# Kernel optimization log

Measured on AMD Instinct MI355X. Metric: run time of the kernel, lower is better.

## Reference

```python
import jax, jax.numpy as jnp
import numpy as np

N_NODES = 50000
N_EDGES = 800000
D_IN = 64
D_HID = 128  # out_channels * expansion(2)
EPS_MSG = 1e-7
EPS_SOFTMAX = 1e-16
EPS_BN = 1e-5
N_LAYERS = 4


def mish(x):
    return x * jnp.tanh(jax.nn.softplus(x))


def setup_inputs() -> dict:
    key = jax.random.key(0)
    ks = jax.random.split(key, 8)
    x = jax.random.normal(ks[0], (N_NODES, D_IN), dtype=jnp.float32)
    edge_index = jax.random.randint(ks[1], (2, N_EDGES), 0, N_NODES, dtype=jnp.int64)
    # Per-layer GENConv MLP params: Linear(64->128), BN(128), ReLU, Linear(128->64)
    s1 = 1.0 / np.sqrt(D_IN)
    s2 = 1.0 / np.sqrt(D_HID)
    W1 = jax.random.uniform(ks[2], (N_LAYERS, D_IN, D_HID), jnp.float32, -s1, s1)
    b1 = jax.random.uniform(ks[3], (N_LAYERS, D_HID), jnp.float32, -s1, s1)
    gamma = jnp.ones((N_LAYERS, D_HID), jnp.float32)
    beta = jnp.zeros((N_LAYERS, D_HID), jnp.float32)
    W2 = jax.random.uniform(ks[4], (N_LAYERS, D_HID, D_IN), jnp.float32, -s2, s2)
    b2 = jax.random.uniform(ks[5], (N_LAYERS, D_IN), jnp.float32, -s2, s2)
    return {"x": x, "edge_index": edge_index, "W1": W1, "b1": b1,
            "gamma": gamma, "beta": beta, "W2": W2, "b2": b2}


def gen_conv(x, src, dst, W1, b1, gamma, beta, W2, b2):
    n = x.shape[0]
    # message: relu(x_j) + eps  -> [E, D]
    msg = jax.nn.relu(x[src]) + EPS_MSG
    # softmax aggregation (t=1) per destination node, per feature channel
    m = jax.ops.segment_max(msg, dst, num_segments=n)
    e = jnp.exp(msg - m[dst])
    denom = jax.ops.segment_sum(e, dst, num_segments=n)[dst] + EPS_SOFTMAX
    alpha = e / denom
    agg = jax.ops.segment_sum(msg * alpha, dst, num_segments=n)
    # residual with destination features, then 2-layer MLP w/ BatchNorm (train mode)
    h = agg + x
    h = h @ W1 + b1
    mu = jnp.mean(h, axis=0)
    var = jnp.var(h, axis=0)  # biased, as torch BN uses for normalization
    h = (h - mu) * jax.lax.rsqrt(var + EPS_BN) * gamma + beta
    h = jax.nn.relu(h)
    return h @ W2 + b2


def reference(x, edge_index, W1, b1, gamma, beta, W2, b2):
    src, dst = edge_index[0], edge_index[1]
    h = x
    for i in range(N_LAYERS):
        h = gen_conv(h, src, dst, W1[i], b1[i], gamma[i], beta[i], W2[i], b2[i])
        if i < N_LAYERS - 1:
            h = mish(h)
    return h
```

## Files before the change

### kernel.cpp

```cpp
#include <hip/hip_runtime.h>
#include <math.h>

#define N_NODES 50000
#define N_EDGES 800000
#define D_IN 64
#define D_HID 128
#define SCAN_B 256
#define N_SB ((N_NODES + SCAN_B - 1) / SCAN_B)
#define NPB 256
#define NB ((N_NODES + NPB - 1) / NPB)
#define P1_BLOCKS 256
#define EPB (N_EDGES / P1_BLOCKS)

typedef unsigned short u16;
typedef unsigned int u32;
typedef __attribute__((ext_vector_type(8))) short short8;
typedef __attribute__((ext_vector_type(4))) float f32x4;

union U4S8 { uint4 u; short8 s; };

__device__ __forceinline__ float bf2f(u16 u) {
    u32 x = ((u32)u) << 16;
    float f; __builtin_memcpy(&f, &x, 4); return f;
}
__device__ __forceinline__ u16 f2bf(float f) {
    u32 x; __builtin_memcpy(&x, &f, 4);
    x += 0x7fffu + ((x >> 16) & 1u);
    return (u16)(x >> 16);
}
__device__ __forceinline__ u32 pk2(float a, float b) {
    return (u32)f2bf(a) | ((u32)f2bf(b) << 16);
}
__device__ __forceinline__ u32 relu2(u32 w) {
    u32 b = (w >> 15) & 0x00010001u;
    u32 m01 = b ^ 0x00010001u;
    u32 M = (m01 << 16) - m01;
    return w & M;
}


__global__ void count_kernel(const int* __restrict__ dst, int* __restrict__ deg, int E) {
    int i = blockIdx.x * blockDim.x + threadIdx.x;
    if (i < E) atomicAdd(&deg[dst[i]], 1);
}

__global__ __launch_bounds__(SCAN_B) void scan_reduce_kernel(const int* __restrict__ deg,
                                                             int* __restrict__ bsum) {
    __shared__ int s[SCAN_B];
    int i = blockIdx.x * SCAN_B + threadIdx.x;
    int v = (i < N_NODES) ? deg[i] : 0;
    s[threadIdx.x] = v;
    __syncthreads();
    #pragma unroll
    for (int o = SCAN_B / 2; o > 0; o >>= 1) {
        if (threadIdx.x < o) s[threadIdx.x] += s[threadIdx.x + o];
        __syncthreads();
    }
    if (threadIdx.x == 0) bsum[blockIdx.x] = s[0];
}

__global__ __launch_bounds__(SCAN_B) void scan_sums_kernel(const int* __restrict__ bsum,
                                                           int* __restrict__ boff) {
    __shared__ int s[SCAN_B];
    int t = threadIdx.x;
    int v = (t < N_SB) ? bsum[t] : 0;
    s[t] = v;
    __syncthreads();
    #pragma unroll
    for (int o = 1; o < SCAN_B; o <<= 1) {
        int u = (t >= o) ? s[t - o] : 0;
        __syncthreads();
        s[t] += u;
        __syncthreads();
    }
    if (t < N_SB) boff[t] = s[t] - v;
}

__global__ __launch_bounds__(SCAN_B) void scan_write_kernel(const int* __restrict__ deg,
                                                            const int* __restrict__ boff,
                                                            int* __restrict__ off) {
    __shared__ int s[SCAN_B];
    int t = threadIdx.x;
    int i = blockIdx.x * SCAN_B + t;
    int v = (i < N_NODES) ? deg[i] : 0;
    s[t] = v;
    __syncthreads();
    #pragma unroll
    for (int o = 1; o < SCAN_B; o <<= 1) {
        int u = (t >= o) ? s[t - o] : 0;
        __syncthreads();
        s[t] += u;
        __syncthreads();
    }
    int incl = s[t] + boff[blockIdx.x];
    if (i < N_NODES) off[i] = incl - v;
    if (i == N_NODES - 1) off[N_NODES] = incl;
}

__global__ void bin_init_kernel(const int* __restrict__ off, int* __restrict__ gcur,
                                int* __restrict__ esrc) {
    int b = threadIdx.x;
    if (b < NB) gcur[b] = off[min(b * NPB, N_NODES)];
    if (b < 16) esrc[N_EDGES + b] = 0;
}

__global__ __launch_bounds__(256) void bin_pass1_kernel(const int* __restrict__ src,
                                                        const int* __restrict__ dst,
                                                        int* __restrict__ gcur,
                                                        int2* __restrict__ ebuf) {
    __shared__ int hist[NB];
    __shared__ int base[NB];
    const int tid = threadIdx.x;
    const int e0 = blockIdx.x * EPB, e1 = e0 + EPB;
    for (int b = tid; b < NB; b += 256) hist[b] = 0;
    __syncthreads();
    for (int i = e0 + tid; i < e1; i += 256)
        atomicAdd(&hist[dst[i] >> 8], 1);
    __syncthreads();
    for (int b = tid; b < NB; b += 256) {
        base[b] = atomicAdd(&gcur[b], hist[b]);
        hist[b] = 0;
    }
    __syncthreads();
    for (int i = e0 + tid; i < e1; i += 256) {
        int d = dst[i];
        int b = d >> 8;
        int slot = base[b] + atomicAdd(&hist[b], 1);
        ebuf[slot] = make_int2(src[i], d);
    }
}

__global__ __launch_bounds__(256) void bin_pass2_kernel(const int* __restrict__ off,
                                                        const int2* __restrict__ ebuf,
                                                        int* __restrict__ esrc) {
    __shared__ int soff[NPB];
    __shared__ int cur[NPB];
    const int b = blockIdx.x;
    const int tid = threadIdx.x;
    const int n0 = b * NPB;
    soff[tid] = off[min(n0 + tid, N_NODES)];
    cur[tid] = 0;
    __syncthreads();
    const int e0 = soff[0];
    const int e1 = off[min(n0 + NPB, N_NODES)];
    for (int i = e0 + tid; i < e1; i += 256) {
        int2 p = ebuf[i];
        int dl = p.y - n0;
        int slot = soff[dl] + atomicAdd(&cur[dl], 1);
        esrc[slot] = p.x;
    }
}

__global__ __launch_bounds__(256) void xcvt_kernel(const float* __restrict__ x,
                                                   u16* __restrict__ xb,
                                                   u16* __restrict__ rb) {
    int i = blockIdx.x * 256 + threadIdx.x;
    if (i < N_NODES * D_IN / 4) {
        float4 v = ((const float4*)x)[i];
        u32 lo = pk2(v.x, v.y), hi = pk2(v.z, v.w);
        ((uint2*)xb)[i] = make_uint2(lo, hi);
        ((uint2*)rb)[i] = make_uint2(relu2(lo), relu2(hi));
    }
}

__global__ __launch_bounds__(256) void wprep_kernel(const float* __restrict__ W1,
                                                    const float* __restrict__ W2,
                                                    u16* __restrict__ w1f,
                                                    u16* __restrict__ w2f) {
    const int b = blockIdx.x;
    const int L = b >> 1;
    if ((b & 1) == 0) {
        const float* W = W1 + (size_t)L * 64 * 128;
        u16* outp = w1f + (size_t)L * 8192;
        for (int idx = threadIdx.x; idx < 1024; idx += 256) {
            int ln = idx & 63, th = idx >> 6;
            int half = th & 1, t = th >> 1;
            int k0 = half * 32 + (ln >> 4) * 8;
            int n = t * 16 + (ln & 15);
            uint4 o;
            o.x = pk2(W[(k0 + 0) * 128 + n], W[(k0 + 1) * 128 + n]);
            o.y = pk2(W[(k0 + 2) * 128 + n], W[(k0 + 3) * 128 + n]);
            o.z = pk2(W[(k0 + 4) * 128 + n], W[(k0 + 5) * 128 + n]);
            o.w = pk2(W[(k0 + 6) * 128 + n], W[(k0 + 7) * 128 + n]);
            *(uint4*)&outp[(size_t)idx * 8] = o;
        }
    } else {
        const float* W = W2 + (size_t)L * 128 * 64;
        u16* outp = w2f + (size_t)L * 8192;
        for (int idx = threadIdx.x; idx < 1024; idx += 256) {
            int ln = idx & 63, th = idx >> 6;
            int ks = th & 3, t = th >> 2;
            int k0 = ks * 32 + (ln >> 4) * 8;
            int n = t * 16 + (ln & 15);
            uint4 o;
            o.x = pk2(W[(k0 + 0) * 64 + n], W[(k0 + 1) * 64 + n]);
            o.y = pk2(W[(k0 + 2) * 64 + n], W[(k0 + 3) * 64 + n]);
            o.z = pk2(W[(k0 + 4) * 64 + n], W[(k0 + 5) * 64 + n]);
            o.w = pk2(W[(k0 + 6) * 64 + n], W[(k0 + 7) * 64 + n]);
            *(uint4*)&outp[(size_t)idx * 8] = o;
        }
    }
}

__global__ __launch_bounds__(256) void agg_kernel(const u16* __restrict__ xb,
                                                  const u16* __restrict__ rb,
                                                  const int* __restrict__ off,
                                                  const int* __restrict__ esrc,
                                                  u16* __restrict__ h) {
    const int node = blockIdx.x * 4 + (threadIdx.x >> 6);
    const int ln = threadIdx.x & 63;
    const int jb = __builtin_amdgcn_readfirstlane(off[node]);
    const int je = __builtin_amdgcn_readfirstlane(off[node + 1]);
    const float xown = bf2f(xb[(size_t)node * 64 + ln]);
    float s0 = 0.f, s1 = 0.f, t0 = 0.f, t1 = 0.f;
    int j = jb;
    const int nfull = (je - jb) >> 4;
    for (int it = 0; it < nfull; ++it, j += 16) {
        #pragma unroll
        for (int kk = 0; kk < 16; kk += 2) {
            int i0 = esrc[j + kk];
            int i1 = esrc[j + kk + 1];
            float m0 = bf2f(rb[(size_t)i0 * 64 + ln]);
            float m1 = bf2f(rb[(size_t)i1 * 64 + ln]);
            float p0 = __expf(m0);
            float p1 = __expf(m1);
            s0 += p0; t0 = fmaf(m0, p0, t0);
            s1 += p1; t1 = fmaf(m1, p1, t1);
        }
    }
    const int rem = je - j;
    if (rem > 0) {
        #pragma unroll
        for (int kk = 0; kk < 16; kk += 2) {
            int i0 = esrc[j + kk];
            int i1 = esrc[j + kk + 1];
            float m0 = bf2f(rb[(size_t)i0 * 64 + ln]);
            float m1 = bf2f(rb[(size_t)i1 * 64 + ln]);
            float p0 = (kk < rem)     ? __expf(m0) : 0.f;
            float p1 = (kk + 1 < rem) ? __expf(m1) : 0.f;
            s0 += p0; t0 = fmaf(m0, p0, t0);
            s1 += p1; t1 = fmaf(m1, p1, t1);
        }
    }
    const float s = s0 + s1, t = t0 + t1;
    const float v = t / (s + 1e-16f) + 1e-7f + xown;
    h[(size_t)node * 64 + ln] = f2bf(v);
}

#define SC1 136
__global__ __launch_bounds__(256) void gemm1_kernel(const u16* __restrict__ A,
                                                    const u16* __restrict__ Wf,
                                                    const float* __restrict__ bias,
                                                    u16* __restrict__ Bout,
                                                    float* __restrict__ S,
                                                    float* __restrict__ Q) {
    __shared__ u16 sC[64 * SC1];
    __shared__ float sRed[2][4][128];
    const int tid = threadIdx.x;
    const int wave = tid >> 6, ln = tid & 63;
    const int lm = ln & 15, quad = ln >> 4;
    const int row0g = blockIdx.x * 64;
    const int row0 = row0g + wave * 16;
    const int rA = min(row0 + lm, N_NODES - 1);

    U4S8 a0, a1;
    a0.u = *(const uint4*)&A[(size_t)rA * 64 + quad * 8];
    a1.u = *(const uint4*)&A[(size_t)rA * 64 + 32 + quad * 8];

    f32x4 acc[8];
    #pragma unroll
    for (int t = 0; t < 8; t++) {
        float b = bias[t * 16 + lm];
        acc[t] = (f32x4){b, b, b, b};
    }
    #pragma unroll
    for (int t = 0; t < 8; t++) {
        U4S8 b0, b1;
        b0.u = *(const uint4*)&Wf[(size_t)((t * 2 + 0) * 64 + ln) * 8];
        b1.u = *(const uint4*)&Wf[(size_t)((t * 2 + 1) * 64 + ln) * 8];
        acc[t] = __builtin_amdgcn_mfma_f32_16x16x32_bf16(a0.s, b0.s, acc[t], 0, 0, 0);
        acc[t] = __builtin_amdgcn_mfma_f32_16x16x32_bf16(a1.s, b1.s, acc[t], 0, 0, 0);
    }
    const int rbase = row0 + quad * 4;
    #pragma unroll
    for (int t = 0; t < 8; t++) {
        float ss = 0.f, qq = 0.f;
        #pragma unroll
        for (int rg = 0; rg < 4; rg++) {
            if (rbase + rg < N_NODES) {
                float v = acc[t][rg];
                ss += v; qq = fmaf(v, v, qq);
            }
        }
        ss += __shfl_xor(ss, 16); ss += __shfl_xor(ss, 32);
        qq += __shfl_xor(qq, 16); qq += __shfl_xor(qq, 32);
        if (quad == 0) {
            sRed[0][wave][t * 16 + lm] = ss;
            sRed[1][wave][t * 16 + lm] = qq;
        }
    }
    const int lr0 = wave * 16 + quad * 4;
    #pragma unroll
    for (int t = 0; t < 8; t++) {
        #pragma unroll
        for (int rg = 0; rg < 4; rg++)
            sC[(lr0 + rg) * SC1 + t * 16 + lm] = f2bf(acc[t][rg]);
    }
    __syncthreads();
    const int c8 = (tid & 15) * 8;
    #pragma unroll
    for (int i = 0; i < 4; i++) {
        int lr = (tid >> 4) + i * 16;
        int r = row0g + lr;
        if (r < N_NODES)
            *(uint4*)&Bout[(size_t)r * 128 + c8] = *(const uint4*)&sC[lr * SC1 + c8];
    }
    if (tid < 128) {
        float v = sRed[0][0][tid] + sRed[0][1][tid] + sRed[0][2][tid] + sRed[0][3][tid];
        atomicAdd(&S[tid], v);
    } else {
        int c = tid - 128;
        float v = sRed[1][0][c] + sRed[1][1][c] + sRed[1][2][c] + sRed[1][3][c];
        atomicAdd(&Q[c], v);
    }
}

__device__ __forceinline__ float mish_f(float v) {
    if (v > 30.f) return v;
    float u = __expf(v);
    float t = (u + 1.f) * (u + 1.f);
    return v * (t - 1.f) / (t + 1.f);
}

#define SC2B 72
#define SC2F 68
__global__ __launch_bounds__(256) void gemm2_kernel(const u16* __restrict__ H,
                                                    const float* __restrict__ S,
                                                    const float* __restrict__ Q,
                                                    const float* __restrict__ gamma,
                                                    const float* __restrict__ beta,
                                                    const u16* __restrict__ Wf,
                                                    const float* __restrict__ bias,
                                                    float* __restrict__ outf,
                                                    u16* __restrict__ xb,
                                                    u16* __restrict__ rb,
                                                    int dobf16) {
    __shared__ float sss[256];
    __shared__ __align__(16) char sCraw[64 * SC2F * 4];
    u16* sCb = (u16*)sCraw;
    float* sCf = (float*)sCraw;
    const int tid = threadIdx.x;
    if (tid < 128) {
        float mean = S[tid] * (1.f / N_NODES);
        float var = fmaxf(Q[tid] * (1.f / N_NODES) - mean * mean, 0.f);
        float sc = gamma[tid] * rsqrtf(var + 1e-5f);
        sss[tid] = sc;
        sss[128 + tid] = beta[tid] - mean * sc;
    }
    __syncthreads();
    const int wave = tid >> 6, ln = tid & 63;
    const int lm = ln & 15, quad = ln >> 4;
    const int row0g = blockIdx.x * 64;
    const int row0 = row0g + wave * 16;
    const int rA = min(row0 + lm, N_NODES - 1);

    f32x4 acc[4];
    #pragma unroll
    for (int t = 0; t < 4; t++) {
        float b = bias[t * 16 + lm];
        acc[t] = (f32x4){b, b, b, b};
    }
    #pragma unroll
    for (int ks = 0; ks < 4; ks++) {
        const int k0 = ks * 32 + quad * 8;
        U4S8 h8;
        h8.u = *(const uint4*)&H[(size_t)rA * 128 + k0];
        U4S8 a;
        #pragma unroll
        for (int j2 = 0; j2 < 4; j2++) {
            int k = k0 + 2 * j2;
            float v0 = fmaxf(fmaf(bf2f((u16)h8.s[2 * j2]),     sss[k],     sss[128 + k]),     0.f);
            float v1 = fmaxf(fmaf(bf2f((u16)h8.s[2 * j2 + 1]), sss[k + 1], sss[128 + k + 1]), 0.f);
            ((u32*)&a.u)[j2] = pk2(v0, v1);
        }
        #pragma unroll
        for (int t = 0; t < 4; t++) {
            U4S8 b;
            b.u = *(const uint4*)&Wf[(size_t)((t * 4 + ks) * 64 + ln) * 8];
            acc[t] = __builtin_amdgcn_mfma_f32_16x16x32_bf16(a.s, b.s, acc[t], 0, 0, 0);
        }
    }
    const int lr0 = wave * 16 + quad * 4;
    if (dobf16) {
        #pragma unroll
        for (int t = 0; t < 4; t++) {
            #pragma unroll
            for (int rg = 0; rg < 4; rg++)
                sCb[(lr0 + rg) * SC2B + t * 16 + lm] = f2bf(mish_f(acc[t][rg]));
        }
        __syncthreads();
        const int c8 = (tid & 7) * 8;
        #pragma unroll
        for (int i = 0; i < 2; i++) {
            int lr = (tid >> 3) + i * 32;
            int r = row0g + lr;
            if (r < N_NODES) {
                uint4 val = *(const uint4*)&sCb[lr * SC2B + c8];
                *(uint4*)&xb[(size_t)r * 64 + c8] = val;
                uint4 rv;
                rv.x = relu2(val.x); rv.y = relu2(val.y);
                rv.z = relu2(val.z); rv.w = relu2(val.w);
                *(uint4*)&rb[(size_t)r * 64 + c8] = rv;
            }
        }
    } else {
        #pragma unroll
        for (int t = 0; t < 4; t++) {
            #pragma unroll
            for (int rg = 0; rg < 4; rg++)
                sCf[(lr0 + rg) * SC2F + t * 16 + lm] = acc[t][rg];
        }
        __syncthreads();
        const int c8 = (tid & 7) * 8;
        #pragma unroll
        for (int i = 0; i < 2; i++) {
            int lr = (tid >> 3) + i * 32;
            int r = row0g + lr;
            if (r < N_NODES) {
                *(float4*)&outf[(size_t)r * 64 + c8]     = *(const float4*)&sCf[lr * SC2F + c8];
                *(float4*)&outf[(size_t)r * 64 + c8 + 4] = *(const float4*)&sCf[lr * SC2F + c8 + 4];
            }
        }
    }
}


extern "C" void kernel_launch(void* const* d_in, const int* in_sizes, int n_in,
                              void* d_out, int out_size, void* d_ws, size_t ws_size,
                              hipStream_t stream) {
    const float* x     = (const float*)d_in[0];
    const int*   ei    = (const int*)d_in[1];
    const float* W1    = (const float*)d_in[2];
    const float* b1    = (const float*)d_in[3];
    const float* gamma = (const float*)d_in[4];
    const float* beta  = (const float*)d_in[5];
    const float* W2    = (const float*)d_in[6];
    const float* b2    = (const float*)d_in[7];
    float* out = (float*)d_out;

    const int* src = ei;
    const int* dst = ei + N_EDGES;

    char* base = (char*)d_ws;
    size_t o = 0;
    auto take = [&](size_t bytes) -> char* {
        char* p = base + o;
        o = (o + bytes + 255) & ~(size_t)255;
        return p;
    };
    int* deg     = (int*)take((size_t)N_NODES * 4);
    int* off     = (int*)take((size_t)(N_NODES + 1) * 4);
    int* esrc    = (int*)take((size_t)(N_EDGES + 16) * 4);
    int2* ebuf   = (int2*)take((size_t)N_EDGES * 8);
    int* bsum    = (int*)take((size_t)N_SB * 4);
    int* boff    = (int*)take((size_t)N_SB * 4);
    int* gcur    = (int*)take((size_t)NB * 4);
    float* bn    = (float*)take(1024 * 4);
    u16* w1f     = (u16*)take((size_t)4 * 8192 * 2);
    u16* w2f     = (u16*)take((size_t)4 * 8192 * 2);
    u16* xbuf    = (u16*)take((size_t)N_NODES * D_IN * 2);
    u16* rbuf    = (u16*)take((size_t)N_NODES * D_IN * 2);
    u16* hbuf    = (u16*)take((size_t)N_NODES * D_IN * 2);
    u16* h1buf   = (u16*)take((size_t)N_NODES * D_HID * 2);

    hipMemsetAsync(deg, 0, (size_t)N_NODES * 4, stream);
    hipMemsetAsync(bn, 0, 1024 * 4, stream);
    count_kernel<<<(N_EDGES + 255) / 256, 256, 0, stream>>>(dst, deg, N_EDGES);
    scan_reduce_kernel<<<N_SB, SCAN_B, 0, stream>>>(deg, bsum);
    scan_sums_kernel<<<1, SCAN_B, 0, stream>>>(bsum, boff);
    scan_write_kernel<<<N_SB, SCAN_B, 0, stream>>>(deg, boff, off);
    bin_init_kernel<<<1, 256, 0, stream>>>(off, gcur, esrc);
    bin_pass1_kernel<<<P1_BLOCKS, 256, 0, stream>>>(src, dst, gcur, ebuf);
    bin_pass2_kernel<<<NB, 256, 0, stream>>>(off, ebuf, esrc);
    xcvt_kernel<<<(N_NODES * D_IN / 4 + 255) / 256, 256, 0, stream>>>(x, xbuf, rbuf);
    wprep_kernel<<<8, 256, 0, stream>>>(W1, W2, w1f, w2f);

    const int NBLK = (N_NODES + 63) / 64;
    const int ABLK = (N_NODES + 3) / 4;
    for (int L = 0; L < 4; L++) {
        float* Sb = bn + L * 256;
        float* Qb = Sb + 128;
        agg_kernel<<<ABLK, 256, 0, stream>>>(xbuf, rbuf, off, esrc, hbuf);
        gemm1_kernel<<<NBLK, 256, 0, stream>>>(
            hbuf, w1f + (size_t)L * 8192, b1 + (size_t)L * D_HID, h1buf,
            Sb, Qb);
        gemm2_kernel<<<NBLK, 256, 0, stream>>>(
            h1buf, Sb, Qb, gamma + (size_t)L * D_HID, beta + (size_t)L * D_HID,
            w2f + (size_t)L * 8192, b2 + (size_t)L * D_IN,
            out, xbuf, rbuf, (L < 3) ? 1 : 0);
    }
}
```

Before: 400.6 us.

## Fuse neighbor aggregation into first GEMM and pack binning edge pairs

The separate aggregation kernel is merged into the first GEMM kernel. Each wave now aggregates its 16 rows into LDS, and the MFMA operands are read from LDS, so the intermediate bf16 h buffer and one launch per layer are gone. The binning buffer also packs src and dst into a single 32-bit word instead of an int2, halving that scratch traffic. The cost is much less parallelism in the gather: it drops from 12500 small blocks to about 782 blocks with serial per-wave node loops. That could hurt latency hiding for the random row gathers.

New measurement: 416.6 us. 4.0% more time.

```diff
diff --git a/kernel.cpp b/kernel.cpp
--- a/kernel.cpp
+++ b/kernel.cpp
@@ -107,7 +107,7 @@
 __global__ __launch_bounds__(256) void bin_pass1_kernel(const int* __restrict__ src,
                                                         const int* __restrict__ dst,
                                                         int* __restrict__ gcur,
-                                                        int2* __restrict__ ebuf) {
+                                                        u32* __restrict__ ebuf) {
     __shared__ int hist[NB];
     __shared__ int base[NB];
     const int tid = threadIdx.x;
@@ -126,12 +126,12 @@
         int d = dst[i];
         int b = d >> 8;
         int slot = base[b] + atomicAdd(&hist[b], 1);
-        ebuf[slot] = make_int2(src[i], d);
+        ebuf[slot] = ((u32)src[i] << 16) | (u32)d;
     }
 }
 
 __global__ __launch_bounds__(256) void bin_pass2_kernel(const int* __restrict__ off,
-                                                        const int2* __restrict__ ebuf,
+                                                        const u32* __restrict__ ebuf,
                                                         int* __restrict__ esrc) {
     __shared__ int soff[NPB];
     __shared__ int cur[NPB];
@@ -144,10 +144,10 @@
     const int e0 = soff[0];
     const int e1 = off[min(n0 + NPB, N_NODES)];
     for (int i = e0 + tid; i < e1; i += 256) {
-        int2 p = ebuf[i];
-        int dl = p.y - n0;
+        u32 p = ebuf[i];
+        int dl = (int)(p & 0xFFFFu) - n0;
         int slot = soff[dl] + atomicAdd(&cur[dl], 1);
-        esrc[slot] = p.x;
+        esrc[slot] = (int)(p >> 16);
     }
 }
 
@@ -202,70 +202,75 @@
     }
 }
 
-__global__ __launch_bounds__(256) void agg_kernel(const u16* __restrict__ xb,
-                                                  const u16* __restrict__ rb,
-                                                  const int* __restrict__ off,
-                                                  const int* __restrict__ esrc,
-                                                  u16* __restrict__ h) {
-    const int node = blockIdx.x * 4 + (threadIdx.x >> 6);
-    const int ln = threadIdx.x & 63;
-    const int jb = __builtin_amdgcn_readfirstlane(off[node]);
-    const int je = __builtin_amdgcn_readfirstlane(off[node + 1]);
-    const float xown = bf2f(xb[(size_t)node * 64 + ln]);
-    float s0 = 0.f, s1 = 0.f, t0 = 0.f, t1 = 0.f;
-    int j = jb;
-    const int nfull = (je - jb) >> 4;
-    for (int it = 0; it < nfull; ++it, j += 16) {
-        #pragma unroll
-        for (int kk = 0; kk < 16; kk += 2) {
-            int i0 = esrc[j + kk];
-            int i1 = esrc[j + kk + 1];
-            float m0 = bf2f(rb[(size_t)i0 * 64 + ln]);
-            float m1 = bf2f(rb[(size_t)i1 * 64 + ln]);
-            float p0 = __expf(m0);
-            float p1 = __expf(m1);
-            s0 += p0; t0 = fmaf(m0, p0, t0);
-            s1 += p1; t1 = fmaf(m1, p1, t1);
-        }
-    }
-    const int rem = je - j;
-    if (rem > 0) {
-        #pragma unroll
-        for (int kk = 0; kk < 16; kk += 2) {
-            int i0 = esrc[j + kk];
-            int i1 = esrc[j + kk + 1];
-            float m0 = bf2f(rb[(size_t)i0 * 64 + ln]);
-            float m1 = bf2f(rb[(size_t)i1 * 64 + ln]);
-            float p0 = (kk < rem)     ? __expf(m0) : 0.f;
-            float p1 = (kk + 1 < rem) ? __expf(m1) : 0.f;
-            s0 += p0; t0 = fmaf(m0, p0, t0);
-            s1 += p1; t1 = fmaf(m1, p1, t1);
-        }
-    }
-    const float s = s0 + s1, t = t0 + t1;
-    const float v = t / (s + 1e-16f) + 1e-7f + xown;
-    h[(size_t)node * 64 + ln] = f2bf(v);
-}
-
+#define SA 72
 #define SC1 136
-__global__ __launch_bounds__(256) void gemm1_kernel(const u16* __restrict__ A,
-                                                    const u16* __restrict__ Wf,
-                                                    const float* __restrict__ bias,
-                                                    u16* __restrict__ Bout,
-                                                    float* __restrict__ S,
-                                                    float* __restrict__ Q) {
+__global__ __launch_bounds__(256) void agg_gemm1_kernel(const u16* __restrict__ xb,
+                                                        const u16* __restrict__ rb,
+                                                        const int* __restrict__ off,
+                                                        const int* __restrict__ esrc,
+                                                        const u16* __restrict__ Wf,
+                                                        const float* __restrict__ bias,
+                                                        u16* __restrict__ Bout,
+                                                        float* __restrict__ S,
+                                                        float* __restrict__ Q) {
+    __shared__ u16 sA[64 * SA];
     __shared__ u16 sC[64 * SC1];
     __shared__ float sRed[2][4][128];
     const int tid = threadIdx.x;
     const int wave = tid >> 6, ln = tid & 63;
+    const int row0g = blockIdx.x * 64;
+
+    for (int i = 0; i < 16; i++) {
+        const int node = row0g + wave * 16 + i;
+        const int lr = wave * 16 + i;
+        if (node < N_NODES) {
+            const int jb = __builtin_amdgcn_readfirstlane(off[node]);
+            const int je = __builtin_amdgcn_readfirstlane(off[node + 1]);
+            const float xown = bf2f(xb[(size_t)node * 64 + ln]);
+            float s0 = 0.f, s1 = 0.f, t0 = 0.f, t1 = 0.f;
+            int j = jb;
+            const int nfull = (je - jb) >> 4;
+            for (int it = 0; it < nfull; ++it, j += 16) {
+                #pragma unroll
+                for (int kk = 0; kk < 16; kk += 2) {
+                    int i0 = esrc[j + kk];
+                    int i1 = esrc[j + kk + 1];
+                    float m0 = bf2f(rb[(size_t)i0 * 64 + ln]);
+                    float m1 = bf2f(rb[(size_t)i1 * 64 + ln]);
+                    float p0 = __expf(m0);
+                    float p1 = __expf(m1);
+                    s0 += p0; t0 = fmaf(m0, p0, t0);
+                    s1 += p1; t1 = fmaf(m1, p1, t1);
+                }
+            }
+            const int rem = je - j;
+            if (rem > 0) {
+                #pragma unroll
+                for (int kk = 0; kk < 16; kk += 2) {
+                    int i0 = esrc[j + kk];
+                    int i1 = esrc[j + kk + 1];
+                    float m0 = bf2f(rb[(size_t)i0 * 64 + ln]);
+                    float m1 = bf2f(rb[(size_t)i1 * 64 + ln]);
+                    float p0 = (kk < rem)     ? __expf(m0) : 0.f;
+                    float p1 = (kk + 1 < rem) ? __expf(m1) : 0.f;
+                    s0 += p0; t0 = fmaf(m0, p0, t0);
+                    s1 += p1; t1 = fmaf(m1, p1, t1);
+                }
+            }
+            const float s = s0 + s1, t = t0 + t1;
+            const float v = t / (s + 1e-16f) + 1e-7f + xown;
+            sA[lr * SA + ln] = f2bf(v);
+        } else {
+            sA[lr * SA + ln] = 0;
+        }
+    }
+
     const int lm = ln & 15, quad = ln >> 4;
-    const int row0g = blockIdx.x * 64;
     const int row0 = row0g + wave * 16;
-    const int rA = min(row0 + lm, N_NODES - 1);
 
     U4S8 a0, a1;
-    a0.u = *(const uint4*)&A[(size_t)rA * 64 + quad * 8];
-    a1.u = *(const uint4*)&A[(size_t)rA * 64 + 32 + quad * 8];
+    a0.u = *(const uint4*)&sA[(wave * 16 + lm) * SA + quad * 8];
+    a1.u = *(const uint4*)&sA[(wave * 16 + lm) * SA + 32 + quad * 8];
 
     f32x4 acc[8];
     #pragma unroll
@@ -461,7 +466,7 @@
     int* deg     = (int*)take((size_t)N_NODES * 4);
     int* off     = (int*)take((size_t)(N_NODES + 1) * 4);
     int* esrc    = (int*)take((size_t)(N_EDGES + 16) * 4);
-    int2* ebuf   = (int2*)take((size_t)N_EDGES * 8);
+    u32* ebuf    = (u32*)take((size_t)N_EDGES * 4);
     int* bsum    = (int*)take((size_t)N_SB * 4);
     int* boff    = (int*)take((size_t)N_SB * 4);
     int* gcur    = (int*)take((size_t)NB * 4);
@@ -470,7 +475,6 @@
     u16* w2f     = (u16*)take((size_t)4 * 8192 * 2);
     u16* xbuf    = (u16*)take((size_t)N_NODES * D_IN * 2);
     u16* rbuf    = (u16*)take((size_t)N_NODES * D_IN * 2);
-    u16* hbuf    = (u16*)take((size_t)N_NODES * D_IN * 2);
     u16* h1buf   = (u16*)take((size_t)N_NODES * D_HID * 2);
 
     hipMemsetAsync(deg, 0, (size_t)N_NODES * 4, stream);
@@ -486,13 +490,12 @@
     wprep_kernel<<<8, 256, 0, stream>>>(W1, W2, w1f, w2f);
 
     const int NBLK = (N_NODES + 63) / 64;
-    const int ABLK = (N_NODES + 3) / 4;
     for (int L = 0; L < 4; L++) {
         float* Sb = bn + L * 256;
         float* Qb = Sb + 128;
-        agg_kernel<<<ABLK, 256, 0, stream>>>(xbuf, rbuf, off, esrc, hbuf);
-        gemm1_kernel<<<NBLK, 256, 0, stream>>>(
-            hbuf, w1f + (size_t)L * 8192, b1 + (size_t)L * D_HID, h1buf,
+        agg_gemm1_kernel<<<NBLK, 256, 0, stream>>>(
+            xbuf, rbuf, off, esrc,
+            w1f + (size_t)L * 8192, b1 + (size_t)L * D_HID, h1buf,
             Sb, Qb);
         gemm2_kernel<<<NBLK, 256, 0, stream>>>(
             h1buf, Sb, Qb, gamma + (size_t)L * D_HID, beta + (size_t)L * D_HID,
```

## Replace two-pass binned CSR build with atomic scatter and merge setup kernels

Applied to the files above, without the earlier changes.

Replaces the three-kernel binned counting sort (bin_init, pass1, pass2 with an int2 staging buffer) with a single scatter kernel that uses per-node atomic cursors initialised during the scan. It also folds the bn memset and esrc padding into count_kernel, and merges the x conversion and weight prep into one launch. The aim is fewer launches and less intermediate memory traffic. In exchange, edge order within each destination becomes nondeterministic and global atomics have poorer locality.

Result: slower. 414.0 us (+3.4%).

```diff
diff --git a/kernel.cpp b/kernel.cpp
--- a/kernel.cpp
+++ b/kernel.cpp
@@ -7,10 +7,7 @@
 #define D_HID 128
 #define SCAN_B 256
 #define N_SB ((N_NODES + SCAN_B - 1) / SCAN_B)
-#define NPB 256
-#define NB ((N_NODES + NPB - 1) / NPB)
-#define P1_BLOCKS 256
-#define EPB (N_EDGES / P1_BLOCKS)
+#define XCVT_B (N_NODES * D_IN / 4 / 256)
 
 typedef unsigned short u16;
 typedef unsigned int u32;
@@ -39,9 +36,15 @@
 }
 
 
-__global__ void count_kernel(const int* __restrict__ dst, int* __restrict__ deg, int E) {
+__global__ void count_kernel(const int* __restrict__ dst, int* __restrict__ deg,
+                             float* __restrict__ bn, int* __restrict__ esrc) {
     int i = blockIdx.x * blockDim.x + threadIdx.x;
-    if (i < E) atomicAdd(&deg[dst[i]], 1);
+    if (i < N_EDGES) atomicAdd(&deg[dst[i]], 1);
+    if (blockIdx.x == 0) {
+        int t = threadIdx.x;
+        ((float4*)bn)[t] = make_float4(0.f, 0.f, 0.f, 0.f);
+        if (t < 16) esrc[N_EDGES + t] = 0;
+    }
 }
 
 __global__ __launch_bounds__(SCAN_B) void scan_reduce_kernel(const int* __restrict__ deg,
@@ -78,7 +81,8 @@
 
 __global__ __launch_bounds__(SCAN_B) void scan_write_kernel(const int* __restrict__ deg,
                                                             const int* __restrict__ boff,
-                                                            int* __restrict__ off) {
+                                                            int* __restrict__ off,
+                                                            int* __restrict__ cur) {
     __shared__ int s[SCAN_B];
     int t = threadIdx.x;
     int i = blockIdx.x * SCAN_B + t;
@@ -93,81 +97,39 @@
         __syncthreads();
     }
     int incl = s[t] + boff[blockIdx.x];
-    if (i < N_NODES) off[i] = incl - v;
+    if (i < N_NODES) {
+        int e = incl - v;
+        off[i] = e;
+        cur[i] = e;
+    }
     if (i == N_NODES - 1) off[N_NODES] = incl;
 }
 
-__global__ void bin_init_kernel(const int* __restrict__ off, int* __restrict__ gcur,
-                                int* __restrict__ esrc) {
-    int b = threadIdx.x;
-    if (b < NB) gcur[b] = off[min(b * NPB, N_NODES)];
-    if (b < 16) esrc[N_EDGES + b] = 0;
-}
-
-__global__ __launch_bounds__(256) void bin_pass1_kernel(const int* __restrict__ src,
-                                                        const int* __restrict__ dst,
-                                                        int* __restrict__ gcur,
-                                                        int2* __restrict__ ebuf) {
-    __shared__ int hist[NB];
-    __shared__ int base[NB];
-    const int tid = threadIdx.x;
-    const int e0 = blockIdx.x * EPB, e1 = e0 + EPB;
-    for (int b = tid; b < NB; b += 256) hist[b] = 0;
-    __syncthreads();
-    for (int i = e0 + tid; i < e1; i += 256)
-        atomicAdd(&hist[dst[i] >> 8], 1);
-    __syncthreads();
-    for (int b = tid; b < NB; b += 256) {
-        base[b] = atomicAdd(&gcur[b], hist[b]);
-        hist[b] = 0;
-    }
-    __syncthreads();
-    for (int i = e0 + tid; i < e1; i += 256) {
-        int d = dst[i];
-        int b = d >> 8;
-        int slot = base[b] + atomicAdd(&hist[b], 1);
-        ebuf[slot] = make_int2(src[i], d);
-    }
-}
-
-__global__ __launch_bounds__(256) void bin_pass2_kernel(const int* __restrict__ off,
-                                                        const int2* __restrict__ ebuf,
-                                                        int* __restrict__ esrc) {
-    __shared__ int soff[NPB];
-    __shared__ int cur[NPB];
-    const int b = blockIdx.x;
-    const int tid = threadIdx.x;
-    const int n0 = b * NPB;
-    soff[tid] = off[min(n0 + tid, N_NODES)];
-    cur[tid] = 0;
-    __syncthreads();
-    const int e0 = soff[0];
-    const int e1 = off[min(n0 + NPB, N_NODES)];
-    for (int i = e0 + tid; i < e1; i += 256) {
-        int2 p = ebuf[i];
-        int dl = p.y - n0;
-        int slot = soff[dl] + atomicAdd(&cur[dl], 1);
-        esrc[slot] = p.x;
-    }
-}
-
-__global__ __launch_bounds__(256) void xcvt_kernel(const float* __restrict__ x,
-                                                   u16* __restrict__ xb,
-                                                   u16* __restrict__ rb) {
-    int i = blockIdx.x * 256 + threadIdx.x;
-    if (i < N_NODES * D_IN / 4) {
+__global__ void scatter_kernel(const int* __restrict__ src, const int* __restrict__ dst,
+                               int* __restrict__ cur, int* __restrict__ esrc) {
+    int i = blockIdx.x * blockDim.x + threadIdx.x;
+    if (i < N_EDGES) {
+        int slot = atomicAdd(&cur[dst[i]], 1);
+        esrc[slot] = src[i];
+    }
+}
+
+__global__ __launch_bounds__(256) void xw_kernel(const float* __restrict__ x,
+                                                 u16* __restrict__ xb,
+                                                 u16* __restrict__ rb,
+                                                 const float* __restrict__ W1,
+                                                 const float* __restrict__ W2,
+                                                 u16* __restrict__ w1f,
+                                                 u16* __restrict__ w2f) {
+    if (blockIdx.x < XCVT_B) {
+        int i = blockIdx.x * 256 + threadIdx.x;
         float4 v = ((const float4*)x)[i];
         u32 lo = pk2(v.x, v.y), hi = pk2(v.z, v.w);
         ((uint2*)xb)[i] = make_uint2(lo, hi);
         ((uint2*)rb)[i] = make_uint2(relu2(lo), relu2(hi));
-    }
-}
-
-__global__ __launch_bounds__(256) void wprep_kernel(const float* __restrict__ W1,
-                                                    const float* __restrict__ W2,
-                                                    u16* __restrict__ w1f,
-                                                    u16* __restrict__ w2f) {
-    const int b = blockIdx.x;
+        return;
+    }
+    const int b = blockIdx.x - XCVT_B;
     const int L = b >> 1;
     if ((b & 1) == 0) {
         const float* W = W1 + (size_t)L * 64 * 128;
@@ -460,11 +422,10 @@
     };
     int* deg     = (int*)take((size_t)N_NODES * 4);
     int* off     = (int*)take((size_t)(N_NODES + 1) * 4);
+    int* cur     = (int*)take((size_t)N_NODES * 4);
     int* esrc    = (int*)take((size_t)(N_EDGES + 16) * 4);
-    int2* ebuf   = (int2*)take((size_t)N_EDGES * 8);
     int* bsum    = (int*)take((size_t)N_SB * 4);
     int* boff    = (int*)take((size_t)N_SB * 4);
-    int* gcur    = (int*)take((size_t)NB * 4);
     float* bn    = (float*)take(1024 * 4);
     u16* w1f     = (u16*)take((size_t)4 * 8192 * 2);
     u16* w2f     = (u16*)take((size_t)4 * 8192 * 2);
@@ -474,16 +435,12 @@
     u16* h1buf   = (u16*)take((size_t)N_NODES * D_HID * 2);
 
     hipMemsetAsync(deg, 0, (size_t)N_NODES * 4, stream);
-    hipMemsetAsync(bn, 0, 1024 * 4, stream);
-    count_kernel<<<(N_EDGES + 255) / 256, 256, 0, stream>>>(dst, deg, N_EDGES);
+    count_kernel<<<(N_EDGES + 255) / 256, 256, 0, stream>>>(dst, deg, bn, esrc);
     scan_reduce_kernel<<<N_SB, SCAN_B, 0, stream>>>(deg, bsum);
     scan_sums_kernel<<<1, SCAN_B, 0, stream>>>(bsum, boff);
-    scan_write_kernel<<<N_SB, SCAN_B, 0, stream>>>(deg, boff, off);
-    bin_init_kernel<<<1, 256, 0, stream>>>(off, gcur, esrc);
-    bin_pass1_kernel<<<P1_BLOCKS, 256, 0, stream>>>(src, dst, gcur, ebuf);
-    bin_pass2_kernel<<<NB, 256, 0, stream>>>(off, ebuf, esrc);
-    xcvt_kernel<<<(N_NODES * D_IN / 4 + 255) / 256, 256, 0, stream>>>(x, xbuf, rbuf);
-    wprep_kernel<<<8, 256, 0, stream>>>(W1, W2, w1f, w2f);
+    scan_write_kernel<<<N_SB, SCAN_B, 0, stream>>>(deg, boff, off, cur);
+    scatter_kernel<<<(N_EDGES + 255) / 256, 256, 0, stream>>>(src, dst, cur, esrc);
+    xw_kernel<<<XCVT_B + 8, 256, 0, stream>>>(x, xbuf, rbuf, W1, W2, w1f, w2f);
 
     const int NBLK = (N_NODES + 63) / 64;
     const int ABLK = (N_NODES + 3) / 4;
```

## Split relu feature buffer into channel halves and aggregate each in a separate pass

Applied to the files above, without the earlier changes.

The relu'd bf16 node features are stored as two 32-channel planar buffers. Aggregation runs in two passes, each wave handling two edges at a time over 32 channels, so each gather touches a smaller working set that fits cache better. The change also packs the binned edge pairs into 32-bit words, fuses the bin-init, memset, x-convert and weight-prep launches into existing kernels, and folds gcur setup into the scan. The cost is twice as many aggregation launches and repeated reads of the CSR index arrays.

Measured after the change: 465.9 us. 1.16x slower.

```diff
diff --git a/kernel.cpp b/kernel.cpp
--- a/kernel.cpp
+++ b/kernel.cpp
@@ -11,6 +11,7 @@
 #define NB ((N_NODES + NPB - 1) / NPB)
 #define P1_BLOCKS 256
 #define EPB (N_EDGES / P1_BLOCKS)
+#define XCVT_B (N_NODES * D_IN / 4 / 256)
 
 typedef unsigned short u16;
 typedef unsigned int u32;
@@ -39,9 +40,15 @@
 }
 
 
-__global__ void count_kernel(const int* __restrict__ dst, int* __restrict__ deg, int E) {
+__global__ void count_kernel(const int* __restrict__ dst, int* __restrict__ deg,
+                             float* __restrict__ bn, int* __restrict__ esrc) {
     int i = blockIdx.x * blockDim.x + threadIdx.x;
-    if (i < E) atomicAdd(&deg[dst[i]], 1);
+    if (i < N_EDGES) atomicAdd(&deg[dst[i]], 1);
+    if (blockIdx.x == 0) {
+        int t = threadIdx.x;
+        ((float4*)bn)[t] = make_float4(0.f, 0.f, 0.f, 0.f);
+        if (t < 16) esrc[N_EDGES + t] = 0;
+    }
 }
 
 __global__ __launch_bounds__(SCAN_B) void scan_reduce_kernel(const int* __restrict__ deg,
@@ -78,7 +85,8 @@
 
 __global__ __launch_bounds__(SCAN_B) void scan_write_kernel(const int* __restrict__ deg,
                                                             const int* __restrict__ boff,
-                                                            int* __restrict__ off) {
+                                                            int* __restrict__ off,
+                                                            int* __restrict__ gcur) {
     __shared__ int s[SCAN_B];
     int t = threadIdx.x;
     int i = blockIdx.x * SCAN_B + t;
@@ -95,19 +103,13 @@
     int incl = s[t] + boff[blockIdx.x];
     if (i < N_NODES) off[i] = incl - v;
     if (i == N_NODES - 1) off[N_NODES] = incl;
-}
-
-__global__ void bin_init_kernel(const int* __restrict__ off, int* __restrict__ gcur,
-                                int* __restrict__ esrc) {
-    int b = threadIdx.x;
-    if (b < NB) gcur[b] = off[min(b * NPB, N_NODES)];
-    if (b < 16) esrc[N_EDGES + b] = 0;
+    if (t == 0) gcur[blockIdx.x] = boff[blockIdx.x];
 }
 
 __global__ __launch_bounds__(256) void bin_pass1_kernel(const int* __restrict__ src,
                                                         const int* __restrict__ dst,
                                                         int* __restrict__ gcur,
-                                                        int2* __restrict__ ebuf) {
+                                                        u32* __restrict__ ebuf) {
     __shared__ int hist[NB];
     __shared__ int base[NB];
     const int tid = threadIdx.x;
@@ -126,12 +128,12 @@
         int d = dst[i];
         int b = d >> 8;
         int slot = base[b] + atomicAdd(&hist[b], 1);
-        ebuf[slot] = make_int2(src[i], d);
+        ebuf[slot] = ((u32)src[i] << 16) | (u32)d;
     }
 }
 
 __global__ __launch_bounds__(256) void bin_pass2_kernel(const int* __restrict__ off,
-                                                        const int2* __restrict__ ebuf,
+                                                        const u32* __restrict__ ebuf,
                                                         int* __restrict__ esrc) {
     __shared__ int soff[NPB];
     __shared__ int cur[NPB];
@@ -144,30 +146,36 @@
     const int e0 = soff[0];
     const int e1 = off[min(n0 + NPB, N_NODES)];
     for (int i = e0 + tid; i < e1; i += 256) {
-        int2 p = ebuf[i];
-        int dl = p.y - n0;
+        u32 p = ebuf[i];
+        int dl = (int)(p & 0xFFFFu) - n0;
         int slot = soff[dl] + atomicAdd(&cur[dl], 1);
-        esrc[slot] = p.x;
-    }
-}
-
-__global__ __launch_bounds__(256) void xcvt_kernel(const float* __restrict__ x,
-                                                   u16* __restrict__ xb,
-                                                   u16* __restrict__ rb) {
-    int i = blockIdx.x * 256 + threadIdx.x;
-    if (i < N_NODES * D_IN / 4) {
+        esrc[slot] = (int)(p >> 16);
+    }
+}
+
+__global__ __launch_bounds__(256) void xw_kernel(const float* __restrict__ x,
+                                                 u16* __restrict__ xb,
+                                                 u16* __restrict__ rbA,
+                                                 u16* __restrict__ rbB,
+                                                 const float* __restrict__ W1,
+                                                 const float* __restrict__ W2,
+                                                 u16* __restrict__ w1f,
+                                                 u16* __restrict__ w2f) {
+    if (blockIdx.x < XCVT_B) {
+        int i = blockIdx.x * 256 + threadIdx.x;
         float4 v = ((const float4*)x)[i];
+        int node = i >> 4;
+        int c4 = (i & 15) * 4;
         u32 lo = pk2(v.x, v.y), hi = pk2(v.z, v.w);
         ((uint2*)xb)[i] = make_uint2(lo, hi);
-        ((uint2*)rb)[i] = make_uint2(relu2(lo), relu2(hi));
-    }
-}
-
-__global__ __launch_bounds__(256) void wprep_kernel(const float* __restrict__ W1,
-                                                    const float* __restrict__ W2,
-                                                    u16* __restrict__ w1f,
-                                                    u16* __restrict__ w2f) {
-    const int b = blockIdx.x;
+        uint2 rv = make_uint2(relu2(lo), relu2(hi));
+        if (c4 < 32)
+            *(uint2*)&rbA[(size_t)node * 32 + c4] = rv;
+        else
+            *(uint2*)&rbB[(size_t)node * 32 + (c4 - 32)] = rv;
+        return;
+    }
+    const int b = blockIdx.x - XCVT_B;
     const int L = b >> 1;
     if ((b & 1) == 0) {
         const float* W = W1 + (size_t)L * 64 * 128;
@@ -202,49 +210,67 @@
     }
 }
 
-__global__ __launch_bounds__(256) void agg_kernel(const u16* __restrict__ xb,
-                                                  const u16* __restrict__ rb,
-                                                  const int* __restrict__ off,
-                                                  const int* __restrict__ esrc,
-                                                  u16* __restrict__ h) {
+__global__ __launch_bounds__(256) void agg32_kernel(const u16* __restrict__ xb,
+                                                    const u16* __restrict__ rh,
+                                                    const int* __restrict__ off,
+                                                    const int* __restrict__ esrc,
+                                                    u16* __restrict__ h,
+                                                    int chbase) {
     const int node = blockIdx.x * 4 + (threadIdx.x >> 6);
     const int ln = threadIdx.x & 63;
+    const int ch = ln & 31;
+    const bool hi = ln >= 32;
     const int jb = __builtin_amdgcn_readfirstlane(off[node]);
     const int je = __builtin_amdgcn_readfirstlane(off[node + 1]);
-    const float xown = bf2f(xb[(size_t)node * 64 + ln]);
-    float s0 = 0.f, s1 = 0.f, t0 = 0.f, t1 = 0.f;
+    float s = 0.f, t = 0.f;
     int j = jb;
-    const int nfull = (je - jb) >> 4;
-    for (int it = 0; it < nfull; ++it, j += 16) {
-        #pragma unroll
-        for (int kk = 0; kk < 16; kk += 2) {
-            int i0 = esrc[j + kk];
-            int i1 = esrc[j + kk + 1];
-            float m0 = bf2f(rb[(size_t)i0 * 64 + ln]);
-            float m1 = bf2f(rb[(size_t)i1 * 64 + ln]);
-            float p0 = __expf(m0);
-            float p1 = __expf(m1);
-            s0 += p0; t0 = fmaf(m0, p0, t0);
-            s1 += p1; t1 = fmaf(m1, p1, t1);
-        }
+    const int nfull = (je - jb) >> 3;
+    for (int it = 0; it < nfull; ++it, j += 8) {
+        int e0 = esrc[j + 0], e1 = esrc[j + 1], e2 = esrc[j + 2], e3 = esrc[j + 3];
+        int e4 = esrc[j + 4], e5 = esrc[j + 5], e6 = esrc[j + 6], e7 = esrc[j + 7];
+        int iA = hi ? e1 : e0;
+        int iB = hi ? e3 : e2;
+        int iC = hi ? e5 : e4;
+        int iD = hi ? e7 : e6;
+        float mA = bf2f(rh[(size_t)iA * 32 + ch]);
+        float mB = bf2f(rh[(size_t)iB * 32 + ch]);
+        float mC = bf2f(rh[(size_t)iC * 32 + ch]);
+        float mD = bf2f(rh[(size_t)iD * 32 + ch]);
+        float pA = __expf(mA), pB = __expf(mB), pC = __expf(mC), pD = __expf(mD);
+        s += pA; t = fmaf(mA, pA, t);
+        s += pB; t = fmaf(mB, pB, t);
+        s += pC; t = fmaf(mC, pC, t);
+        s += pD; t = fmaf(mD, pD, t);
     }
     const int rem = je - j;
     if (rem > 0) {
-        #pragma unroll
-        for (int kk = 0; kk < 16; kk += 2) {
-            int i0 = esrc[j + kk];
-            int i1 = esrc[j + kk + 1];
-            float m0 = bf2f(rb[(size_t)i0 * 64 + ln]);
-            float m1 = bf2f(rb[(size_t)i1 * 64 + ln]);
-            float p0 = (kk < rem)     ? __expf(m0) : 0.f;
-            float p1 = (kk + 1 < rem) ? __expf(m1) : 0.f;
-            s0 += p0; t0 = fmaf(m0, p0, t0);
-            s1 += p1; t1 = fmaf(m1, p1, t1);
-        }
-    }
-    const float s = s0 + s1, t = t0 + t1;
-    const float v = t / (s + 1e-16f) + 1e-7f + xown;
-    h[(size_t)node * 64 + ln] = f2bf(v);
+        int e0 = esrc[j + 0], e1 = esrc[j + 1], e2 = esrc[j + 2], e3 = esrc[j + 3];
+        int e4 = esrc[j + 4], e5 = esrc[j + 5], e6 = esrc[j + 6], e7 = esrc[j + 7];
+        const int sl = hi ? 1 : 0;
+        int iA = hi ? e1 : e0;
+        int iB = hi ? e3 : e2;
+        int iC = hi ? e5 : e4;
+        int iD = hi ? e7 : e6;
+        float mA = bf2f(rh[(size_t)iA * 32 + ch]);
+        float mB = bf2f(rh[(size_t)iB * 32 + ch]);
+        float mC = bf2f(rh[(size_t)iC * 32 + ch]);
+        float mD = bf2f(rh[(size_t)iD * 32 + ch]);
+        float pA = (sl     < rem) ? __expf(mA) : 0.f;
+        float pB = (sl + 2 < rem) ? __expf(mB) : 0.f;
+        float pC = (sl + 4 < rem) ? __expf(mC) : 0.f;
+        float pD = (sl + 6 < rem) ? __expf(mD) : 0.f;
+        s += pA; t = fmaf(mA, pA, t);
+        s += pB; t = fmaf(mB, pB, t);
+        s += pC; t = fmaf(mC, pC, t);
+        s += pD; t = fmaf(mD, pD, t);
+    }
+    s += __shfl_xor(s, 32);
+    t += __shfl_xor(t, 32);
+    if (!hi) {
+        float xown = bf2f(xb[(size_t)node * 64 + chbase + ch]);
+        float v = t / (s + 1e-16f) + 1e-7f + xown;
+        h[(size_t)node * 64 + chbase + ch] = f2bf(v);
+    }
 }
 
 #define SC1 136
@@ -343,7 +369,8 @@
                                                     const float* __restrict__ bias,
                                                     float* __restrict__ outf,
                                                     u16* __restrict__ xb,
-                                                    u16* __restrict__ rb,
+                                                    u16* __restrict__ rbA,
+                                                    u16* __restrict__ rbB,
                                                     int dobf16) {
     __shared__ float sss[256];
     __shared__ __align__(16) char sCraw[64 * SC2F * 4];
@@ -410,7 +437,10 @@
                 uint4 rv;
                 rv.x = relu2(val.x); rv.y = relu2(val.y);
                 rv.z = relu2(val.z); rv.w = relu2(val.w);
-                *(uint4*)&rb[(size_t)r * 64 + c8] = rv;
+                if (c8 < 32)
+                    *(uint4*)&rbA[(size_t)r * 32 + c8] = rv;
+                else
+                    *(uint4*)&rbB[(size_t)r * 32 + (c8 - 32)] = rv;
             }
         }
     } else {
@@ -461,7 +491,7 @@
     int* deg     = (int*)take((size_t)N_NODES * 4);
     int* off     = (int*)take((size_t)(N_NODES + 1) * 4);
     int* esrc    = (int*)take((size_t)(N_EDGES + 16) * 4);
-    int2* ebuf   = (int2*)take((size_t)N_EDGES * 8);
+    u32* ebuf    = (u32*)take((size_t)N_EDGES * 4);
     int* bsum    = (int*)take((size_t)N_SB * 4);
     int* boff    = (int*)take((size_t)N_SB * 4);
     int* gcur    = (int*)take((size_t)NB * 4);
@@ -469,34 +499,33 @@
     u16* w1f     = (u16*)take((size_t)4 * 8192 * 2);
     u16* w2f     = (u16*)take((size_t)4 * 8192 * 2);
     u16* xbuf    = (u16*)take((size_t)N_NODES * D_IN * 2);
-    u16* rbuf    = (u16*)take((size_t)N_NODES * D_IN * 2);
+    u16* rbA     = (u16*)take((size_t)N_NODES * 32 * 2);
+    u16* rbB     = (u16*)take((size_t)N_NODES * 32 * 2);
     u16* hbuf    = (u16*)take((size_t)N_NODES * D_IN * 2);
     u16* h1buf   = (u16*)take((size_t)N_NODES * D_HID * 2);
 
     hipMemsetAsync(deg, 0, (size_t)N_NODES * 4, stream);
-    hipMemsetAsync(bn, 0, 1024 * 4, stream);
-    count_kernel<<<(N_EDGES + 255) / 256, 256, 0, stream>>>(dst, deg, N_EDGES);
+    count_kernel<<<(N_EDGES + 255) / 256, 256, 0, stream>>>(dst, deg, bn, esrc);
     scan_reduce_kernel<<<N_SB, SCAN_B, 0, stream>>>(deg, bsum);
     scan_sums_kernel<<<1, SCAN_B, 0, stream>>>(bsum, boff);
-    scan_write_kernel<<<N_SB, SCAN_B, 0, stream>>>(deg, boff, off);
-    bin_init_kernel<<<1, 256, 0, stream>>>(off, gcur, esrc);
+    scan_write_kernel<<<N_SB, SCAN_B, 0, stream>>>(deg, boff, off, gcur);
     bin_pass1_kernel<<<P1_BLOCKS, 256, 0, stream>>>(src, dst, gcur, ebuf);
     bin_pass2_kernel<<<NB, 256, 0, stream>>>(off, ebuf, esrc);
-    xcvt_kernel<<<(N_NODES * D_IN / 4 + 255) / 256, 256, 0, stream>>>(x, xbuf, rbuf);
-    wprep_kernel<<<8, 256, 0, stream>>>(W1, W2, w1f, w2f);
+    xw_kernel<<<XCVT_B + 8, 256, 0, stream>>>(x, xbuf, rbA, rbB, W1, W2, w1f, w2f);
 
     const int NBLK = (N_NODES + 63) / 64;
     const int ABLK = (N_NODES + 3) / 4;
     for (int L = 0; L < 4; L++) {
         float* Sb = bn + L * 256;
         float* Qb = Sb + 128;
-        agg_kernel<<<ABLK, 256, 0, stream>>>(xbuf, rbuf, off, esrc, hbuf);
+        agg32_kernel<<<ABLK, 256, 0, stream>>>(xbuf, rbA, off, esrc, hbuf, 0);
+        agg32_kernel<<<ABLK, 256, 0, stream>>>(xbuf, rbB, off, esrc, hbuf, 32);
         gemm1_kernel<<<NBLK, 256, 0, stream>>>(
             hbuf, w1f + (size_t)L * 8192, b1 + (size_t)L * D_HID, h1buf,
             Sb, Qb);
         gemm2_kernel<<<NBLK, 256, 0, stream>>>(
             h1buf, Sb, Qb, gamma + (size_t)L * D_HID, beta + (size_t)L * D_HID,
             w2f + (size_t)L * 8192, b2 + (size_t)L * D_IN,
-            out, xbuf, rbuf, (L < 3) ? 1 : 0);
-    }
-}
+            out, xbuf, rbA, rbB, (L < 3) ? 1 : 0);
+    }
+}
```
